# Kernel optimization log

Measured on AMD Instinct MI355X. Metric: run time of the kernel, lower is better.

The kernel has to match this reference:

```python
import jax, jax.numpy as jnp
import numpy as np

EMBED_DIM = 768
NUM_HEADS = 12
HEAD_DIM = EMBED_DIM // NUM_HEADS


def setup_inputs() -> dict:
    key = jax.random.key(0)
    k_x, k_wqkv, k_bqkv, k_wo, k_bo = jax.random.split(key, 5)
    B, S = 2, 4096
    x = jax.random.normal(k_x, (B, S, EMBED_DIM), dtype=jnp.float32)
    # nn.Linear default init: U(-1/sqrt(fan_in), 1/sqrt(fan_in))
    bound = 1.0 / np.sqrt(EMBED_DIM)
    w_qkv = jax.random.uniform(k_wqkv, (EMBED_DIM, 3 * EMBED_DIM), jnp.float32, -bound, bound)
    b_qkv = jax.random.uniform(k_bqkv, (3 * EMBED_DIM,), jnp.float32, -bound, bound)
    w_out = jax.random.uniform(k_wo, (EMBED_DIM, EMBED_DIM), jnp.float32, -bound, bound)
    b_out = jax.random.uniform(k_bo, (EMBED_DIM,), jnp.float32, -bound, bound)
    return {"x": x, "w_qkv": w_qkv, "b_qkv": b_qkv, "w_out": w_out, "b_out": b_out}


def reference(x, w_qkv, b_qkv, w_out, b_out):
    B, S, E = x.shape
    H, D = NUM_HEADS, HEAD_DIM
    qkv = x @ w_qkv + b_qkv                       # [B,S,3E]
    qkv = qkv.reshape(B, S, 3, H, D)
    q = qkv[:, :, 0].transpose(0, 2, 1, 3)        # [B,H,S,D]
    k = qkv[:, :, 1].transpose(0, 2, 1, 3)
    v = qkv[:, :, 2].transpose(0, 2, 1, 3)
    scores = jnp.einsum('bhqd,bhkd->bhqk', q, k) / jnp.sqrt(jnp.float32(D))
    causal = jnp.tril(jnp.ones((S, S), dtype=bool))
    scores = jnp.where(causal, scores, -jnp.inf)
    weights = jax.nn.softmax(scores, axis=-1)
    attended = jnp.einsum('bhqk,bhkd->bhqd', weights, v)  # [B,H,S,D]
    attended = attended.transpose(0, 2, 1, 3).reshape(B, S, E)
    return attended @ w_out + b_out
```

## Files before the change

kernel.cpp:

```cpp
#include <hip/hip_runtime.h>

#define EMBED 768
#define NH 12
#define HD 64
#define SEQ 4096
#define BATCH 2
#define MROWS (BATCH * SEQ)
#define N3E (3 * EMBED)

typedef short bf16x8 __attribute__((ext_vector_type(8)));
typedef float fx4 __attribute__((ext_vector_type(4)));
typedef float f32x16 __attribute__((ext_vector_type(16)));
typedef unsigned short ushort_t;
typedef unsigned short us4 __attribute__((ext_vector_type(4)));

#if __has_builtin(__builtin_amdgcn_exp2f)
#define EXP2F(x) __builtin_amdgcn_exp2f(x)
#else
#define EXP2F(x) exp2f(x)
#endif

#define QSCALE 0.18033688011112042f

__device__ inline ushort_t f2bf(float f) {
  union { float f; unsigned int u; } x; x.f = f;
  unsigned int r = x.u + 0x7fffu + ((x.u >> 16) & 1u);
  return (ushort_t)(r >> 16);
}

__device__ inline unsigned int cvtpk(float a, float b) {
  unsigned int r;
  asm("v_cvt_pk_bf16_f32 %0, %1, %2" : "=v"(r) : "v"(a), "v"(b));
  return r;
}
__device__ inline void plswap(unsigned int& x, unsigned int& y) {
  asm("v_permlane32_swap_b32 %0, %1" : "+v"(x), "+v"(y));
}

__global__ __launch_bounds__(256) void convert_x(const float* __restrict__ in,
                                                 ushort_t* __restrict__ out) {
  int i = (blockIdx.x * 256 + threadIdx.x) * 8;
  float4 a = *(const float4*)(in + i);
  float4 b = *(const float4*)(in + i + 4);
  bf16x8 o;
  o[0] = f2bf(a.x); o[1] = f2bf(a.y); o[2] = f2bf(a.z); o[3] = f2bf(a.w);
  o[4] = f2bf(b.x); o[5] = f2bf(b.y); o[6] = f2bf(b.z); o[7] = f2bf(b.w);
  *(bf16x8*)(out + i) = o;
}

__global__ __launch_bounds__(256) void transpose_w(const float* __restrict__ in,
                                                   ushort_t* __restrict__ out,
                                                   int K, int N) {
  __shared__ float t[64][65];
  const int bn = blockIdx.x * 64, bk = blockIdx.y * 64;
  const int c = threadIdx.x & 63, r0 = threadIdx.x >> 6;
#pragma unroll
  for (int rr = 0; rr < 16; ++rr) {
    int row = rr * 4 + r0;
    t[row][c] = in[(size_t)(bk + row) * N + bn + c];
  }
  __syncthreads();
#pragma unroll
  for (int rr = 0; rr < 16; ++rr) {
    int row = rr * 4 + r0;
    out[(size_t)(bn + row) * K + bk + c] = f2bf(t[c][row]);
  }
}

template <int N_, int K_, bool SCATTER>
__global__ __launch_bounds__(256) void gemm_mfma(
    const ushort_t* __restrict__ A, const ushort_t* __restrict__ Bt,
    const float* __restrict__ bias, float* __restrict__ outF,
    ushort_t* __restrict__ oq, ushort_t* __restrict__ ok,
    ushort_t* __restrict__ ov) {
  constexpr int NT = K_ / 32;
  __shared__ __align__(16) ushort_t smem[24576];
  ushort_t* As_ = smem;
  ushort_t* Bs_ = smem + 12288;
  const int tid = threadIdx.x;
  const int w = tid >> 6, lane = tid & 63;
  const int quad = lane >> 4, ln = lane & 15;

  const int gx = gridDim.x;
  const int nwg = gx * gridDim.y;
  int lin = blockIdx.y * gx + blockIdx.x;
  lin = (lin & 7) * (nwg >> 3) + (lin >> 3);
  const int bm = (lin / gx) * 128, bn = (lin % gx) * 128;

  const int wm = (w >> 1) * 64, wn = (w & 1) * 64;
  const int sr = lane >> 2;
  const int sslot = lane & 3;

  auto STAGE = [&](int ti, int b) {
#pragma unroll
    for (int r = 0; r < 2; ++r) {
      const int c = w + r * 4;
      const int m = c * 16 + sr;
      const int kk = ti * 32 + ((sslot ^ (m & 3)) << 3);
      __builtin_amdgcn_global_load_lds(
          (const __attribute__((address_space(1))) unsigned int*)
              (A + (size_t)(bm + m) * K_ + kk),
          (__attribute__((address_space(3))) unsigned int*)(As_ + b * 4096 + c * 512),
          16, 0, 0);
      __builtin_amdgcn_global_load_lds(
          (const __attribute__((address_space(1))) unsigned int*)
              (Bt + (size_t)(bn + m) * K_ + kk),
          (__attribute__((address_space(3))) unsigned int*)(Bs_ + b * 4096 + c * 512),
          16, 0, 0);
    }
  };

  fx4 acc[4][4] = {};

  auto COMPUTE = [&](int b) {
    bf16x8 af[4], bfr[4];
#pragma unroll
    for (int i = 0; i < 4; ++i) {
      const int m = wm + i * 16 + ln;
      af[i] = *(const bf16x8*)(As_ + b * 4096 + m * 32 + ((quad ^ (m & 3)) << 3));
    }
#pragma unroll
    for (int j = 0; j < 4; ++j) {
      const int n = wn + j * 16 + ln;
      bfr[j] = *(const bf16x8*)(Bs_ + b * 4096 + n * 32 + ((quad ^ (n & 3)) << 3));
    }
#pragma unroll
    for (int i = 0; i < 4; ++i)
#pragma unroll
      for (int j = 0; j < 4; ++j)
        acc[i][j] = __builtin_amdgcn_mfma_f32_16x16x32_bf16(af[i], bfr[j],
                                                            acc[i][j], 0, 0, 0);
  };

  STAGE(0, 0);
  STAGE(1, 1);

  int bufR = 0;
  for (int t = 0; t < NT - 2; ++t) {
    asm volatile("s_waitcnt vmcnt(4)" ::: "memory");
    __builtin_amdgcn_s_barrier();
    __builtin_amdgcn_sched_barrier(0);
    const int bufS = (bufR >= 1) ? bufR - 1 : 2;
    STAGE(t + 2, bufS);
    COMPUTE(bufR);
    bufR = (bufR < 2) ? bufR + 1 : 0;
  }
  asm volatile("s_waitcnt vmcnt(4)" ::: "memory");
  __builtin_amdgcn_s_barrier();
  __builtin_amdgcn_sched_barrier(0);
  COMPUTE(bufR);
  bufR = (bufR < 2) ? bufR + 1 : 0;
  asm volatile("s_waitcnt vmcnt(0)" ::: "memory");
  __builtin_amdgcn_s_barrier();
  __builtin_amdgcn_sched_barrier(0);
  COMPUTE(bufR);

  if (!SCATTER) {
#pragma unroll
    for (int j = 0; j < 4; ++j) {
      const int n = bn + wn + j * 16 + ln;
      const float bv = bias[n];
#pragma unroll
      for (int i = 0; i < 4; ++i) {
        const int m0 = bm + wm + i * 16 + quad * 4;
#pragma unroll
        for (int r = 0; r < 4; ++r)
          outF[(size_t)(m0 + r) * N_ + n] = acc[i][j][r] + bv;
      }
    }
  } else {
    const int t3 = bn / EMBED;
    if (t3 == 2) {
      __syncthreads();
#pragma unroll
      for (int j = 0; j < 4; ++j) {
        const int nl = wn + j * 16 + ln;
        const float bv = bias[bn + nl];
        const int key = (nl & 7) << 4;
#pragma unroll
        for (int i = 0; i < 4; ++i) {
          const int m0 = wm + i * 16 + quad * 4;
#pragma unroll
          for (int r = 0; r < 4; ++r)
            smem[nl * 128 + ((m0 + r) ^ key)] = f2bf(acc[i][j][r] + bv);
        }
      }
      __syncthreads();
      const int b_ = bm >> 12, s0 = bm & 4095;
      const int lr = lane >> 4;
      const int lc = lane & 15;
#pragma unroll
      for (int it = 0; it < 8; ++it) {
        const int nl = w * 32 + it * 4 + lr;
        const int rem = bn + nl - 2 * EMBED;
        const int h = rem >> 6, d = rem & 63;
        const int mc = lc * 8;
        bf16x8 val =
            *(const bf16x8*)&smem[nl * 128 + (mc ^ ((nl & 7) << 4))];
        *(bf16x8*)&ov[((size_t)(b_ * NH + h) * HD + d) * SEQ + s0 + mc] = val;
      }
    } else {
#pragma unroll
      for (int j = 0; j < 4; ++j) {
        const int nn = bn + wn + j * 16 + ln;
        const int rem = nn - t3 * EMBED;
        const int h = rem >> 6, d = rem & 63;
        const float bv = bias[nn];
#pragma unroll
        for (int i = 0; i < 4; ++i) {
          const int m0 = bm + wm + i * 16 + quad * 4;
#pragma unroll
          for (int r = 0; r < 4; ++r) {
            const int m = m0 + r;
            const int b_ = m >> 12, s = m & 4095;
            const float v = acc[i][j][r] + bv;
            if (t3 == 0)
              oq[((size_t)(b_ * NH + h) * SEQ + s) * HD + d] = f2bf(v * QSCALE);
            else
              ok[((size_t)(b_ * NH + h) * SEQ + s) * HD + d] = f2bf(v);
          }
        }
      }
    }
  }
}

__global__ __launch_bounds__(256, 4) void flash_mfma(
    const ushort_t* __restrict__ qb, const ushort_t* __restrict__ kb,
    const ushort_t* __restrict__ vb, ushort_t* __restrict__ attn) {
  __shared__ __align__(16) ushort_t Ks[2][64 * 64];
  __shared__ __align__(16) ushort_t Vt[2][64 * 64];

  const int tid = threadIdx.x;
  const int w = tid >> 6;
  const int lane = tid & 63;
  const int r32 = lane & 31;
  const int hf = lane >> 5;
  const int gk = r32 & 7;
  const int rc4 = hf * 4;

  const int bh = blockIdx.x;
  const int y = blockIdx.y;
  const int qt2 = (y < 11) ? (31 - y) : (y - 11);
  const int ktd0 = 2 * qt2;
  const int nkt = 2 * qt2 + 2;

  const size_t base = (size_t)bh * SEQ * HD;
  const ushort_t* Qg = qb + base;
  const ushort_t* Kg = kb + base;
  const ushort_t* Vg = vb + base;

  const int srow = lane >> 3;
  const int sg = (lane & 7) ^ srow;
  const int row0 = w * 8 + srow;
  const ushort_t* kp = Kg + (size_t)row0 * HD + (sg << 3);
  const ushort_t* vp = Vg + (size_t)row0 * SEQ + (sg << 3);

  const int qoff = w * 32 + r32;
  const int qglob = qt2 * 128 + qoff;
  bf16x8 qf[4];
  {
    const ushort_t* qrow = Qg + (size_t)qglob * HD;
#pragma unroll
    for (int dc = 0; dc < 4; ++dc)
      qf[dc] = *(const bf16x8*)(qrow + dc * 16 + hf * 8);
  }

  f32x16 oacc[2] = {};
  float lsum = 0.f;

#pragma unroll
  for (int r2 = 0; r2 < 2; ++r2) {
    __builtin_amdgcn_global_load_lds(
        (const __attribute__((address_space(1))) unsigned int*)(kp + r2 * (32 * HD)),
        (__attribute__((address_space(3))) unsigned int*)(&Ks[0][(w + r2 * 4) * 512]),
        16, 0, 0);
    __builtin_amdgcn_global_load_lds(
        (const __attribute__((address_space(1))) unsigned int*)(vp + r2 * (32 * SEQ)),
        (__attribute__((address_space(3))) unsigned int*)(&Vt[0][(w + r2 * 4) * 512]),
        16, 0, 0);
  }
  kp += 64 * HD;
  vp += 64;

  for (int kt = 0; kt < nkt; ++kt) {
    const int cur = kt & 1;
    __syncthreads();
    if (kt + 1 < nkt) {
      const int nxt = cur ^ 1;
#pragma unroll
      for (int r2 = 0; r2 < 2; ++r2) {
        __builtin_amdgcn_global_load_lds(
            (const __attribute__((address_space(1))) unsigned int*)(kp + r2 * (32 * HD)),
            (__attribute__((address_space(3))) unsigned int*)(&Ks[nxt][(w + r2 * 4) * 512]),
            16, 0, 0);
        __builtin_amdgcn_global_load_lds(
            (const __attribute__((address_space(1))) unsigned int*)(vp + r2 * (32 * SEQ)),
            (__attribute__((address_space(3))) unsigned int*)(&Vt[nxt][(w + r2 * 4) * 512]),
            16, 0, 0);
      }
      kp += 64 * HD;
      vp += 64;
    }

    const bool diag = (kt >= ktd0);
    const int kbase0 = (kt == ktd0) ? 0 : 64;

#pragma unroll
    for (int krb = 0; krb < 2; ++krb) {
      const int krow = (krb * 32 + r32) * 64;
      f32x16 s = {};
#pragma unroll
      for (int dc = 0; dc < 4; ++dc) {
        bf16x8 kf =
            *(const bf16x8*)(&Ks[cur][krow + (((2 * dc + hf) ^ gk) << 3)]);
        s = __builtin_amdgcn_mfma_f32_32x32x16_bf16(kf, qf[dc], s, 0, 0, 0);
      }
      if (diag) {
        const int kb2 = kbase0 + krb * 32;
#pragma unroll
        for (int r = 0; r < 16; ++r) {
          const int rowc = (r & 3) + 8 * (r >> 2) + rc4;
          if (kb2 + rowc > qoff) s[r] = -1e30f;
        }
      }
      float e[16];
#pragma unroll
      for (int r = 0; r < 16; ++r) {
        e[r] = EXP2F(s[r]);
        lsum += e[r];
      }
#pragma unroll
      for (int ch = 0; ch < 2; ++ch) {
        const int rb = ch * 8;
        unsigned int x0 = cvtpk(e[rb + 0], e[rb + 1]);
        unsigned int x1 = cvtpk(e[rb + 2], e[rb + 3]);
        unsigned int y0 = cvtpk(e[rb + 4], e[rb + 5]);
        unsigned int y1 = cvtpk(e[rb + 6], e[rb + 7]);
        plswap(x0, y0);
        plswap(x1, y1);
        union { unsigned int u[4]; bf16x8 v; } pf;
        pf.u[0] = x0; pf.u[1] = x1; pf.u[2] = y0; pf.u[3] = y1;
        const int c = 2 * krb + ch;
        __builtin_amdgcn_s_setprio(1);
#pragma unroll
        for (int vb2 = 0; vb2 < 2; ++vb2) {
          const int vrow = (vb2 * 32 + r32) * 64;
          bf16x8 vf =
              *(const bf16x8*)(&Vt[cur][vrow + (((2 * c + hf) ^ gk) << 3)]);
          oacc[vb2] =
              __builtin_amdgcn_mfma_f32_32x32x16_bf16(vf, pf.v, oacc[vb2], 0, 0, 0);
        }
        __builtin_amdgcn_s_setprio(0);
      }
    }
  }

  lsum += __shfl_xor(lsum, 32);
  const float inv = 1.f / lsum;
  const int b_ = bh / NH, h = bh % NH;
  ushort_t* orow = attn + (size_t)(b_ * SEQ + qglob) * EMBED + h * HD;
#pragma unroll
  for (int vb2 = 0; vb2 < 2; ++vb2)
#pragma unroll
    for (int rq = 0; rq < 4; ++rq) {
      us4 o;
#pragma unroll
      for (int r = 0; r < 4; ++r) o[r] = f2bf(oacc[vb2][rq * 4 + r] * inv);
      *(us4*)(orow + vb2 * 32 + rq * 8 + rc4) = o;
    }
}

extern "C" void kernel_launch(void* const* d_in, const int* in_sizes, int n_in,
                              void* d_out, int out_size, void* d_ws,
                              size_t ws_size, hipStream_t stream) {
  const float* x = (const float*)d_in[0];
  const float* w_qkv = (const float*)d_in[1];
  const float* b_qkv = (const float*)d_in[2];
  const float* w_out = (const float*)d_in[3];
  const float* b_out = (const float*)d_in[4];
  float* out = (float*)d_out;

  const size_t per = (size_t)BATCH * NH * SEQ * HD;
  ushort_t* q_buf = (ushort_t*)d_ws;
  ushort_t* k_buf = q_buf + per;
  ushort_t* v_buf = k_buf + per;
  ushort_t* attn_buf = v_buf + per;
  ushort_t* xb = attn_buf + per;
  ushort_t* wqkvT = xb + per;
  ushort_t* woutT = wqkvT + (size_t)N3E * EMBED;

  convert_x<<<(MROWS * EMBED) / 2048, 256, 0, stream>>>(x, xb);
  transpose_w<<<dim3(N3E / 64, EMBED / 64), 256, 0, stream>>>(w_qkv, wqkvT,
                                                              EMBED, N3E);
  transpose_w<<<dim3(EMBED / 64, EMBED / 64), 256, 0, stream>>>(w_out, woutT,
                                                                EMBED, EMBED);

  dim3 g1(N3E / 128, MROWS / 128);
  gemm_mfma<N3E, EMBED, true><<<g1, 256, 0, stream>>>(
      xb, wqkvT, b_qkv, nullptr, q_buf, k_buf, v_buf);

  dim3 g2(BATCH * NH, 32);
  flash_mfma<<<g2, 256, 0, stream>>>(q_buf, k_buf, v_buf, attn_buf);

  dim3 g3(EMBED / 128, MROWS / 128);
  gemm_mfma<EMBED, EMBED, false><<<g3, 256, 0, stream>>>(
      attn_buf, woutT, b_out, out, nullptr, nullptr, nullptr);
}
```

Before: 229.3 us.

## Split flash attention warps over query and key halves with LDS reduction

Re-partitions the 4 warps of the flash attention kernel so each warp handles 64 query rows (two 32-row MFMA blocks) against one 32-key half of each tile, instead of 32 query rows against the full 64-key tile. Each K/V fragment loaded from LDS now feeds two MFMAs, and warps whose key half lies entirely above the causal diagonal skip the tile. Partial outputs and row sums from the two key-half warps are combined through LDS at the end. The cost is more accumulator registers (occupancy hint lowered from 4 to 3), an epilogue reduction with extra syncs, and load imbalance on diagonal tiles.

```diff
diff --git a/kernel.cpp b/kernel.cpp
--- a/kernel.cpp
+++ b/kernel.cpp
@@ -225,11 +225,10 @@
   }
 }
 
-__global__ __launch_bounds__(256, 4) void flash_mfma(
+__global__ __launch_bounds__(256, 3) void flash_mfma(
     const ushort_t* __restrict__ qb, const ushort_t* __restrict__ kb,
     const ushort_t* __restrict__ vb, ushort_t* __restrict__ attn) {
-  __shared__ __align__(16) ushort_t Ks[2][64 * 64];
-  __shared__ __align__(16) ushort_t Vt[2][64 * 64];
+  __shared__ __align__(16) ushort_t smemAll[16896];
 
   const int tid = threadIdx.x;
   const int w = tid >> 6;
@@ -238,6 +237,8 @@
   const int hf = lane >> 5;
   const int gk = r32 & 7;
   const int rc4 = hf * 4;
+  const int qh = w & 1;
+  const int kh = w >> 1;
 
   const int bh = blockIdx.x;
   const int y = blockIdx.y;
@@ -256,28 +257,30 @@
   const ushort_t* kp = Kg + (size_t)row0 * HD + (sg << 3);
   const ushort_t* vp = Vg + (size_t)row0 * SEQ + (sg << 3);
 
-  const int qoff = w * 32 + r32;
-  const int qglob = qt2 * 128 + qoff;
-  bf16x8 qf[4];
+  const int qbase = qt2 * 128 + qh * 64 + r32;
+  bf16x8 qfA[4], qfB[4];
   {
-    const ushort_t* qrow = Qg + (size_t)qglob * HD;
-#pragma unroll
-    for (int dc = 0; dc < 4; ++dc)
-      qf[dc] = *(const bf16x8*)(qrow + dc * 16 + hf * 8);
-  }
-
-  f32x16 oacc[2] = {};
-  float lsum = 0.f;
+    const ushort_t* qra = Qg + (size_t)qbase * HD;
+    const ushort_t* qrb = qra + (size_t)32 * HD;
+#pragma unroll
+    for (int dc = 0; dc < 4; ++dc) {
+      qfA[dc] = *(const bf16x8*)(qra + dc * 16 + hf * 8);
+      qfB[dc] = *(const bf16x8*)(qrb + dc * 16 + hf * 8);
+    }
+  }
+
+  f32x16 oacc[2][2] = {};
+  float lsumA = 0.f, lsumB = 0.f;
 
 #pragma unroll
   for (int r2 = 0; r2 < 2; ++r2) {
     __builtin_amdgcn_global_load_lds(
         (const __attribute__((address_space(1))) unsigned int*)(kp + r2 * (32 * HD)),
-        (__attribute__((address_space(3))) unsigned int*)(&Ks[0][(w + r2 * 4) * 512]),
+        (__attribute__((address_space(3))) unsigned int*)(smemAll + (w + r2 * 4) * 512),
         16, 0, 0);
     __builtin_amdgcn_global_load_lds(
         (const __attribute__((address_space(1))) unsigned int*)(vp + r2 * (32 * SEQ)),
-        (__attribute__((address_space(3))) unsigned int*)(&Vt[0][(w + r2 * 4) * 512]),
+        (__attribute__((address_space(3))) unsigned int*)(smemAll + 8192 + (w + r2 * 4) * 512),
         16, 0, 0);
   }
   kp += 64 * HD;
@@ -292,83 +295,146 @@
       for (int r2 = 0; r2 < 2; ++r2) {
         __builtin_amdgcn_global_load_lds(
             (const __attribute__((address_space(1))) unsigned int*)(kp + r2 * (32 * HD)),
-            (__attribute__((address_space(3))) unsigned int*)(&Ks[nxt][(w + r2 * 4) * 512]),
+            (__attribute__((address_space(3))) unsigned int*)(smemAll + nxt * 4096 + (w + r2 * 4) * 512),
             16, 0, 0);
         __builtin_amdgcn_global_load_lds(
             (const __attribute__((address_space(1))) unsigned int*)(vp + r2 * (32 * SEQ)),
-            (__attribute__((address_space(3))) unsigned int*)(&Vt[nxt][(w + r2 * 4) * 512]),
+            (__attribute__((address_space(3))) unsigned int*)(smemAll + 8192 + nxt * 4096 + (w + r2 * 4) * 512),
             16, 0, 0);
       }
       kp += 64 * HD;
       vp += 64;
     }
 
-    const bool diag = (kt >= ktd0);
-    const int kbase0 = (kt == ktd0) ? 0 : 64;
-
-#pragma unroll
-    for (int krb = 0; krb < 2; ++krb) {
-      const int krow = (krb * 32 + r32) * 64;
-      f32x16 s = {};
-#pragma unroll
-      for (int dc = 0; dc < 4; ++dc) {
-        bf16x8 kf =
-            *(const bf16x8*)(&Ks[cur][krow + (((2 * dc + hf) ^ gk) << 3)]);
-        s = __builtin_amdgcn_mfma_f32_32x32x16_bf16(kf, qf[dc], s, 0, 0, 0);
-      }
-      if (diag) {
-        const int kb2 = kbase0 + krb * 32;
-#pragma unroll
-        for (int r = 0; r < 16; ++r) {
-          const int rowc = (r & 3) + 8 * (r >> 2) + rc4;
-          if (kb2 + rowc > qoff) s[r] = -1e30f;
+    int rel = -64;
+    if (kt >= ktd0) rel = (kt - ktd0) * 64 + kh * 32 - qh * 64;
+    if (rel >= 64) continue;
+
+    const ushort_t* Kc = smemAll + cur * 4096;
+    const ushort_t* Vc = smemAll + 8192 + cur * 4096;
+    const int krow = (kh * 32 + r32) * 64;
+
+    f32x16 sA = {}, sB = {};
+#pragma unroll
+    for (int dc = 0; dc < 4; ++dc) {
+      bf16x8 kf = *(const bf16x8*)(Kc + krow + (((2 * dc + hf) ^ gk) << 3));
+      sA = __builtin_amdgcn_mfma_f32_32x32x16_bf16(kf, qfA[dc], sA, 0, 0, 0);
+      sB = __builtin_amdgcn_mfma_f32_32x32x16_bf16(kf, qfB[dc], sB, 0, 0, 0);
+    }
+    if (rel == 0) {
+#pragma unroll
+      for (int r = 0; r < 16; ++r) {
+        const int rowc = (r & 3) + 8 * (r >> 2) + rc4;
+        if (rowc > r32) sA[r] = -1e30f;
+      }
+    } else if (rel == 32) {
+#pragma unroll
+      for (int r = 0; r < 16; ++r) {
+        const int rowc = (r & 3) + 8 * (r >> 2) + rc4;
+        sA[r] = -1e30f;
+        if (rowc > r32) sB[r] = -1e30f;
+      }
+    }
+    float eA[16], eB[16];
+#pragma unroll
+    for (int r = 0; r < 16; ++r) {
+      eA[r] = EXP2F(sA[r]);
+      eB[r] = EXP2F(sB[r]);
+    }
+    {
+      float a0 = ((eA[0] + eA[1]) + (eA[2] + eA[3])) +
+                 ((eA[4] + eA[5]) + (eA[6] + eA[7]));
+      float a1 = ((eA[8] + eA[9]) + (eA[10] + eA[11])) +
+                 ((eA[12] + eA[13]) + (eA[14] + eA[15]));
+      lsumA += a0 + a1;
+      float b0 = ((eB[0] + eB[1]) + (eB[2] + eB[3])) +
+                 ((eB[4] + eB[5]) + (eB[6] + eB[7]));
+      float b1 = ((eB[8] + eB[9]) + (eB[10] + eB[11])) +
+                 ((eB[12] + eB[13]) + (eB[14] + eB[15]));
+      lsumB += b0 + b1;
+    }
+    __builtin_amdgcn_s_setprio(1);
+#pragma unroll
+    for (int ch = 0; ch < 2; ++ch) {
+      const int rb = ch * 8;
+      unsigned int ax0 = cvtpk(eA[rb + 0], eA[rb + 1]);
+      unsigned int ax1 = cvtpk(eA[rb + 2], eA[rb + 3]);
+      unsigned int ay0 = cvtpk(eA[rb + 4], eA[rb + 5]);
+      unsigned int ay1 = cvtpk(eA[rb + 6], eA[rb + 7]);
+      plswap(ax0, ay0);
+      plswap(ax1, ay1);
+      union { unsigned int u[4]; bf16x8 v; } pfA;
+      pfA.u[0] = ax0; pfA.u[1] = ax1; pfA.u[2] = ay0; pfA.u[3] = ay1;
+      unsigned int bx0 = cvtpk(eB[rb + 0], eB[rb + 1]);
+      unsigned int bx1 = cvtpk(eB[rb + 2], eB[rb + 3]);
+      unsigned int by0 = cvtpk(eB[rb + 4], eB[rb + 5]);
+      unsigned int by1 = cvtpk(eB[rb + 6], eB[rb + 7]);
+      plswap(bx0, by0);
+      plswap(bx1, by1);
+      union { unsigned int u[4]; bf16x8 v; } pfB;
+      pfB.u[0] = bx0; pfB.u[1] = bx1; pfB.u[2] = by0; pfB.u[3] = by1;
+      const int c = kh * 2 + ch;
+#pragma unroll
+      for (int vb2 = 0; vb2 < 2; ++vb2) {
+        bf16x8 vf = *(const bf16x8*)(Vc + (vb2 * 32 + r32) * 64 +
+                                     (((2 * c + hf) ^ gk) << 3));
+        oacc[0][vb2] =
+            __builtin_amdgcn_mfma_f32_32x32x16_bf16(vf, pfA.v, oacc[0][vb2], 0, 0, 0);
+        oacc[1][vb2] =
+            __builtin_amdgcn_mfma_f32_32x32x16_bf16(vf, pfB.v, oacc[1][vb2], 0, 0, 0);
+      }
+    }
+    __builtin_amdgcn_s_setprio(0);
+  }
+
+  lsumA += __shfl_xor(lsumA, 32);
+  lsumB += __shfl_xor(lsumB, 32);
+  __syncthreads();
+  float* ored = (float*)smemAll;
+  float* lred = (float*)(smemAll + 16384);
+  if (kh == 1) {
+    float* ob = ored + qh * 4096;
+#pragma unroll
+    for (int qc = 0; qc < 2; ++qc)
+#pragma unroll
+      for (int vb2 = 0; vb2 < 2; ++vb2)
+#pragma unroll
+        for (int r = 0; r < 16; ++r)
+          ob[((qc * 2 + vb2) * 16 + r) * 64 + lane] = oacc[qc][vb2][r];
+    lred[qh * 128 + lane] = lsumA;
+    lred[qh * 128 + 64 + lane] = lsumB;
+  }
+  __syncthreads();
+  if (kh == 0) {
+    float* ob = ored + qh * 4096;
+#pragma unroll
+    for (int qc = 0; qc < 2; ++qc)
+#pragma unroll
+      for (int vb2 = 0; vb2 < 2; ++vb2)
+#pragma unroll
+        for (int r = 0; r < 16; ++r)
+          oacc[qc][vb2][r] += ob[((qc * 2 + vb2) * 16 + r) * 64 + lane];
+    lsumA += lred[qh * 128 + lane];
+    lsumB += lred[qh * 128 + 64 + lane];
+    const int b_ = bh / NH, h = bh % NH;
+#pragma unroll
+    for (int qc = 0; qc < 2; ++qc) {
+      const float inv = 1.f / (qc ? lsumB : lsumA);
+      ushort_t* orow = attn +
+          (size_t)(b_ * SEQ + qt2 * 128 + qh * 64 + qc * 32 + r32) * EMBED +
+          h * HD;
+#pragma unroll
+      for (int vb2 = 0; vb2 < 2; ++vb2)
+#pragma unroll
+        for (int rq = 0; rq < 4; ++rq) {
+          us4 o;
+#pragma unroll
+          for (int r = 0; r < 4; ++r)
+            o[r] = f2bf(oacc[qc][vb2][rq * 4 + r] * inv);
+          *(us4*)(orow + vb2 * 32 + rq * 8 + rc4) = o;
         }
-      }
-      float e[16];
-#pragma unroll
-      for (int r = 0; r < 16; ++r) {
-        e[r] = EXP2F(s[r]);
-        lsum += e[r];
-      }
-#pragma unroll
-      for (int ch = 0; ch < 2; ++ch) {
-        const int rb = ch * 8;
-        unsigned int x0 = cvtpk(e[rb + 0], e[rb + 1]);
-        unsigned int x1 = cvtpk(e[rb + 2], e[rb + 3]);
-        unsigned int y0 = cvtpk(e[rb + 4], e[rb + 5]);
-        unsigned int y1 = cvtpk(e[rb + 6], e[rb + 7]);
-        plswap(x0, y0);
-        plswap(x1, y1);
-        union { unsigned int u[4]; bf16x8 v; } pf;
-        pf.u[0] = x0; pf.u[1] = x1; pf.u[2] = y0; pf.u[3] = y1;
-        const int c = 2 * krb + ch;
-        __builtin_amdgcn_s_setprio(1);
-#pragma unroll
-        for (int vb2 = 0; vb2 < 2; ++vb2) {
-          const int vrow = (vb2 * 32 + r32) * 64;
-          bf16x8 vf =
-              *(const bf16x8*)(&Vt[cur][vrow + (((2 * c + hf) ^ gk) << 3)]);
-          oacc[vb2] =
-              __builtin_amdgcn_mfma_f32_32x32x16_bf16(vf, pf.v, oacc[vb2], 0, 0, 0);
-        }
-        __builtin_amdgcn_s_setprio(0);
-      }
-    }
-  }
-
-  lsum += __shfl_xor(lsum, 32);
-  const float inv = 1.f / lsum;
-  const int b_ = bh / NH, h = bh % NH;
-  ushort_t* orow = attn + (size_t)(b_ * SEQ + qglob) * EMBED + h * HD;
-#pragma unroll
-  for (int vb2 = 0; vb2 < 2; ++vb2)
-#pragma unroll
-    for (int rq = 0; rq < 4; ++rq) {
-      us4 o;
-#pragma unroll
-      for (int r = 0; r < 4; ++r) o[r] = f2bf(oacc[vb2][rq * 4 + r] * inv);
-      *(us4*)(orow + vb2 * 32 + rq * 8 + rc4) = o;
-    }
+    }
+  }
 }
 
 extern "C" void kernel_launch(void* const* d_in, const int* in_sizes, int n_in,
```

Result: faster. 223.0 us (-2.8%).
